# Optimization experiments

Hardware: AMD Instinct MI355X
Metric: run time of the kernel (lower is better)

## Reference

```python
import jax, jax.numpy as jnp
import numpy as np

N = 50000
E = 1600000
F_IN = 256
DIMS = 64
N_CLS = 16
R = 8


def glorot(key, shape):
    fan = shape[-2] + shape[-1] if len(shape) >= 2 else shape[-1] * 2
    std = jnp.sqrt(6.0 / fan)
    return jax.random.uniform(key, shape, jnp.float32, -std, std)


def setup_inputs() -> dict:
    key = jax.random.key(0)
    ks = jax.random.split(key, 12)
    x = jax.random.normal(ks[0], (N, F_IN), jnp.float32)
    edge_index = jax.random.randint(ks[1], (2, E), 0, N)
    edge_weight = jax.random.uniform(ks[2], (E,), jnp.float32)
    edge_color = jax.random.randint(ks[3], (E,), 0, R)
    W1 = glorot(ks[4], (R, F_IN, DIMS))
    atten1 = glorot(ks[5], (R, 2 * DIMS))
    root1 = glorot(ks[6], (F_IN, DIMS))
    bias1 = jnp.zeros((DIMS,), jnp.float32)
    W2 = glorot(ks[7], (R, DIMS, N_CLS))
    atten2 = glorot(ks[8], (R, 2 * N_CLS))
    root2 = glorot(ks[9], (DIMS, N_CLS))
    bias2 = jnp.zeros((N_CLS,), jnp.float32)
    return dict(x=x, edge_index=edge_index, edge_weight=edge_weight,
                edge_color=edge_color, W1=W1, atten1=atten1, root1=root1,
                bias1=bias1, W2=W2, atten2=atten2, root2=root2, bias2=bias2)


def wrgat_conv(x, src, dst, ew, ec, W, atten, root, bias):
    # x: [N, f_in]; W: [R, f_in, d]; atten: [R, 2d]
    d = W.shape[-1]
    xr = jnp.einsum('nf,rfd->rnd', x, W)            # [R, N, d] per-relation projection
    xi = xr[ec, dst]                                 # [E, d] dst (x_i)
    xj = xr[ec, src]                                 # [E, d] src (x_j)
    a_i = atten[:, :d][ec]                           # [E, d]
    a_j = atten[:, d:][ec]
    s = jnp.sum(a_i * xi + a_j * xj, axis=-1)        # [E]
    s = jax.nn.leaky_relu(s, 0.2)
    # segment softmax over (relation, destination) groups
    seg = ec * N + dst                               # [E], each edge belongs to one relation
    nseg = R * N
    m = jax.ops.segment_max(s, seg, num_segments=nseg)
    m = jnp.where(jnp.isfinite(m), m, 0.0)           # empty segments -> 0
    e = jnp.exp(s - m[seg])
    denom = jax.ops.segment_sum(e, seg, num_segments=nseg)
    alpha = e / jnp.maximum(denom[seg], 1e-16)
    msg = (alpha * ew)[:, None] * xj                 # [E, d]
    summed = jax.ops.segment_sum(msg, seg, num_segments=nseg).reshape(R, N, d)
    cnt = jax.ops.segment_sum(jnp.ones_like(ew), seg, num_segments=nseg).reshape(R, N, 1)
    out = (summed / jnp.maximum(cnt, 1.0)).sum(axis=0)  # mean aggr per relation, summed over relations
    return out + x @ root + bias


def reference(x, edge_index, edge_weight, edge_color, W1, atten1, root1, bias1,
              W2, atten2, root2, bias2):
    src, dst = edge_index[0], edge_index[1]          # PyG flow source_to_target: x_j=src, x_i=dst
    h = wrgat_conv(x, src, dst, edge_weight, edge_color, W1, atten1, root1, bias1)
    h = jax.nn.relu(h)                               # dropout p=0 -> identity
    h = wrgat_conv(h, src, dst, edge_weight, edge_color, W2, atten2, root2, bias2)
    return jax.nn.log_softmax(h, axis=1)
```

## Files before the change

### kernel.cpp

```cpp
#include <hip/hip_runtime.h>
#include <math.h>

#define N_NODES 50000
#define N_EDGES 1600000
#define F_IN    256
#define DIMS    64
#define N_CLS   16
#define R_REL   8
#define CAP     96

#define PROJ_BLKS 3519
#define CSR_BLKS  3125
#define FRONT_BLKS (PROJ_BLKS + CSR_BLKS)

typedef short bf16x8 __attribute__((ext_vector_type(8)));
typedef float f32x4  __attribute__((ext_vector_type(4)));
typedef unsigned int u32;
typedef const __attribute__((address_space(1))) u32* gas_ptr;
typedef __attribute__((address_space(3))) u32* las_ptr;

__device__ __forceinline__ void async16(const void* g, void* l) {
    __builtin_amdgcn_global_load_lds((gas_ptr)g, (las_ptr)l, 16, 0, 0);
}

__device__ __forceinline__ unsigned short f2bf(float f) {
    unsigned u = __float_as_uint(f);
    unsigned r = (u + 0x7fffu + ((u >> 16) & 1u)) >> 16;
    return (unsigned short)r;
}
__device__ __forceinline__ float bf2f(unsigned short u) {
    return __uint_as_float(((unsigned)u) << 16);
}

__global__ __launch_bounds__(256) void cvt_kernel(
        const float* __restrict__ x, ushort* __restrict__ xb,
        const float* __restrict__ W1, const float* __restrict__ root1,
        ushort* __restrict__ wt1) {
    const int bid = blockIdx.x, t = threadIdx.x;
    if (bid < 12500) {
        int i4 = bid * 256 + t;
        float4 v = ((const float4*)x)[i4];
        ushort4 o;
        o.x = f2bf(v.x); o.y = f2bf(v.y); o.z = f2bf(v.z); o.w = f2bf(v.w);
        ((ushort4*)xb)[i4] = o;
    } else {
        int idx = (bid - 12500) * 256 + t;
        int r = idx >> 14, rem = idx & 16383;
        int n = rem >> 8, k = rem & 255;
        float v = (r < 8) ? W1[((size_t)r * F_IN + k) * DIMS + n]
                          : root1[(size_t)k * DIMS + n];
        wt1[idx] = f2bf(v);
    }
}

#define BM 128
__global__ __launch_bounds__(256, 6) void front_kernel(
        const ushort* __restrict__ xb, const ushort* __restrict__ wt1,
        const float* __restrict__ at1,
        ushort* __restrict__ xr1b, float* __restrict__ hroot,
        float* __restrict__ si1, float* __restrict__ sj1,
        const int* __restrict__ ei, const int* __restrict__ ecol,
        const float* __restrict__ ew, int* __restrict__ fill,
        unsigned long long* __restrict__ rec) {
    __shared__ ushort xs[BM * 64];
    const int bid = blockIdx.x;
    const int t = threadIdx.x;

    int pb = -1, cb = -1;
    if (bid < 2 * CSR_BLKS) { if (bid & 1) cb = bid >> 1; else pb = bid >> 1; }
    else pb = CSR_BLKS + (bid - 2 * CSR_BLKS);

    if (cb >= 0) {
        int idx = cb * 256 + t;
        int2  s2 = ((const int2*)ei)[idx];
        int2  d2 = ((const int2*)(ei + N_EDGES))[idx];
        int2  c2 = ((const int2*)ecol)[idx];
        float2 w2 = ((const float2*)ew)[idx];
        int p0 = atomicAdd(&fill[d2.x], 1);
        int p1 = atomicAdd(&fill[d2.y], 1);
        unsigned long long r0 =
            ((unsigned long long)__float_as_uint(w2.x) << 32)
            | (unsigned)(s2.x | (c2.x << 16));
        unsigned long long r1 =
            ((unsigned long long)__float_as_uint(w2.y) << 32)
            | (unsigned)(s2.y | (c2.y << 16));
        int i0 = (p0 < CAP) ? d2.x * CAP + p0 : N_NODES * CAP;
        int i1 = (p1 < CAP) ? d2.y * CAP + p1 : N_NODES * CAP;
        __builtin_nontemporal_store(r0, &rec[i0]);
        __builtin_nontemporal_store(r1, &rec[i1]);
        return;
    }

    const int r = pb / 391;
    const int node0 = (pb % 391) * BM;
    const ushort* wrow = wt1 + (size_t)r * 64 * 256;

    const int w = t >> 6, lane = t & 63;
    const int lane15 = lane & 15, quad = lane >> 4;
    const int row0 = w * 32 + lane15;
    const int sw0 = row0 & 7;

    f32x4 acc[2][4];
    #pragma unroll
    for (int a = 0; a < 2; ++a)
        #pragma unroll
        for (int b = 0; b < 4; ++b)
            acc[a][b] = (f32x4){0.f, 0.f, 0.f, 0.f};

    for (int s = 0; s < 4; ++s) {
        __syncthreads();
        #pragma unroll
        for (int c = 0; c < 4; ++c) {
            int slot = c * 256 + t;
            int row = slot >> 3, k8p = slot & 7;
            int k8 = k8p ^ (row & 7);
            int node = node0 + row;
            if (node >= N_NODES) node = N_NODES - 1;
            async16(&xb[(size_t)node * 256 + s * 64 + k8 * 8],
                    &xs[(c * 256 + w * 64) * 8]);
        }
        __syncthreads();
        #pragma unroll
        for (int kk = 0; kk < 2; ++kk) {
            int k8 = kk * 4 + quad;
            int aidx = row0 * 64 + ((k8 ^ sw0) << 3);
            bf16x8 a0 = *(const bf16x8*)&xs[aidx];
            bf16x8 a1 = *(const bf16x8*)&xs[aidx + 16 * 64];
            int kg = s * 64 + kk * 32 + quad * 8;
            #pragma unroll
            for (int nt = 0; nt < 4; ++nt) {
                bf16x8 b = *(const bf16x8*)&wrow[(size_t)(nt * 16 + lane15) * 256 + kg];
                acc[0][nt] = __builtin_amdgcn_mfma_f32_16x16x32_bf16(a0, b, acc[0][nt], 0, 0, 0);
                acc[1][nt] = __builtin_amdgcn_mfma_f32_16x16x32_bf16(a1, b, acc[1][nt], 0, 0, 0);
            }
        }
    }

    const float* at = at1 + r * 128;
    #pragma unroll
    for (int mt = 0; mt < 2; ++mt) {
        float pi[4] = {0.f, 0.f, 0.f, 0.f};
        float pj[4] = {0.f, 0.f, 0.f, 0.f};
        #pragma unroll
        for (int nt = 0; nt < 4; ++nt) {
            int gcol = nt * 16 + lane15;
            float ai = 0.f, aj = 0.f;
            if (r < 8) { ai = at[gcol]; aj = at[64 + gcol]; }
            #pragma unroll
            for (int reg = 0; reg < 4; ++reg) {
                float v = acc[mt][nt][reg];
                int grow = node0 + w * 32 + mt * 16 + quad * 4 + reg;
                if (grow < N_NODES) {
                    if (r < 8)
                        xr1b[((size_t)r * N_NODES + grow) * 64 + gcol] = f2bf(v);
                    else
                        hroot[(size_t)grow * 64 + gcol] = v;
                }
                pi[reg] += ai * v;
                pj[reg] += aj * v;
            }
        }
        if (r < 8) {
            #pragma unroll
            for (int reg = 0; reg < 4; ++reg) {
                float s_ = pi[reg], u_ = pj[reg];
                #pragma unroll
                for (int off = 1; off < 16; off <<= 1) {
                    s_ += __shfl_xor(s_, off, 64);
                    u_ += __shfl_xor(u_, off, 64);
                }
                if (lane15 == 0) {
                    int grow = node0 + w * 32 + mt * 16 + quad * 4 + reg;
                    if (grow < N_NODES) {
                        si1[r * N_NODES + grow] = s_;
                        sj1[r * N_NODES + grow] = u_;
                    }
                }
            }
        }
    }
}

__global__ __launch_bounds__(256) void agg1s_kernel(
        const unsigned long long* __restrict__ rec, const int* __restrict__ fill,
        const float* __restrict__ si, const float* __restrict__ sj,
        const ushort* __restrict__ xr1b, const float* __restrict__ hroot,
        const float* __restrict__ bias1, float* __restrict__ h) {
    __shared__ int   esrc[4][CAP];
    __shared__ float ecoef[4][CAP];
    __shared__ float sden[4][8];
    __shared__ int   scnt[4][8];
    __shared__ float ssi[4][8];
    const int t = threadIdx.x;
    const int w = t >> 6, lane = t & 63;
    const int d = blockIdx.x * 4 + w;
    if (lane < 8) {
        sden[w][lane] = 0.f; scnt[w][lane] = 0;
        ssi[w][lane] = si[lane * N_NODES + d];
    }
    const int n = min(fill[d], CAP);
    const int base = d * CAP;
    float ex[2] = {0.f, 0.f}, ww[2] = {0.f, 0.f};
    int cc[2] = {0, 0};
    #pragma unroll
    for (int ii = 0; ii < 2; ++ii) {
        int i = lane + ii * 64;
        if (i < n) {
            unsigned long long rv = rec[base + i];
            int px = (int)(unsigned)rv;
            int s = px & 0xffff, c = (px >> 16) & 0x7fff;
            esrc[w][i] = px;
            float sc = ssi[w][c] + sj[c * N_NODES + s];
            sc = sc > 0.f ? sc : 0.2f * sc;
            float e = __expf(sc);
            ex[ii] = e; cc[ii] = c; ww[ii] = __uint_as_float((unsigned)(rv >> 32));
            atomicAdd(&sden[w][c], e);
            atomicAdd(&scnt[w][c], 1);
        }
    }
    #pragma unroll
    for (int ii = 0; ii < 2; ++ii) {
        int i = lane + ii * 64;
        if (i < n)
            ecoef[w][i] = ex[ii] / fmaxf(sden[w][cc[ii]], 1e-16f)
                          * ww[ii] / (float)scnt[w][cc[ii]];
    }
    const int sub = lane >> 5;
    const int l31 = lane & 31;
    float ax[8] = {0.f,0.f,0.f,0.f,0.f,0.f,0.f,0.f};
    float ay[8] = {0.f,0.f,0.f,0.f,0.f,0.f,0.f,0.f};
    int i0 = 0;
    for (; i0 + 16 <= n; i0 += 16) {
        u32 rv[8]; float cf[8];
        #pragma unroll
        for (int u = 0; u < 8; ++u) {
            int e = i0 + 2 * u + sub;
            int p = esrc[w][e];
            cf[u] = ecoef[w][e];
            int row = (p >> 16) * N_NODES + (p & 0xffff);
            rv[u] = *(const u32*)&xr1b[(size_t)row * 64 + 2 * l31];
        }
        #pragma unroll
        for (int u = 0; u < 8; ++u) {
            ax[u] += cf[u] * bf2f((unsigned short)(rv[u] & 0xffffu));
            ay[u] += cf[u] * bf2f((unsigned short)(rv[u] >> 16));
        }
    }
    for (int e = i0 + sub; e < n; e += 2) {
        int p = esrc[w][e];
        float c = ecoef[w][e];
        int row = (p >> 16) * N_NODES + (p & 0xffff);
        u32 v = *(const u32*)&xr1b[(size_t)row * 64 + 2 * l31];
        ax[0] += c * bf2f((unsigned short)(v & 0xffffu));
        ay[0] += c * bf2f((unsigned short)(v >> 16));
    }
    float sx = ((ax[0] + ax[1]) + (ax[2] + ax[3])) + ((ax[4] + ax[5]) + (ax[6] + ax[7]));
    float sy = ((ay[0] + ay[1]) + (ay[2] + ay[3])) + ((ay[4] + ay[5]) + (ay[6] + ay[7]));
    sx += __shfl_xor(sx, 32, 64);
    sy += __shfl_xor(sy, 32, 64);
    if (sub == 0) {
        float2 hr = *(const float2*)&hroot[(size_t)d * 64 + 2 * l31];
        float2 bi = *(const float2*)&bias1[2 * l31];
        float2 o;
        o.x = fmaxf(sx + hr.x + bi.x, 0.f);
        o.y = fmaxf(sy + hr.y + bi.y, 0.f);
        *(float2*)&h[(size_t)d * 64 + 2 * l31] = o;
    }
}

__global__ __launch_bounds__(256) void proj2_kernel(
        const float* __restrict__ h, const float* __restrict__ W2,
        const float* __restrict__ atten2, const float* __restrict__ root2,
        ushort* __restrict__ xr2b, float* __restrict__ si2,
        float* __restrict__ sj2, float* __restrict__ hroot2) {
    __shared__ float w2sh[8][64][16];
    __shared__ float a2sh[8][32];
    __shared__ float hsh[32][65];
    const int t = threadIdx.x;
    for (int i = t; i < R_REL * DIMS * N_CLS; i += 256)
        w2sh[i >> 10][(i >> 4) & 63][i & 15] = W2[i];
    if (t < R_REL * 2 * N_CLS) a2sh[t >> 5][t & 31] = atten2[t];
    const int node0 = blockIdx.x * 32;
    for (int i = t; i < 32 * 64; i += 256) {
        int nn = i >> 6, kk = i & 63;
        int node = node0 + nn;
        hsh[nn][kk] = (node < N_NODES) ? h[(size_t)node * 64 + kk] : 0.f;
    }
    __syncthreads();
    const int nl = t & 31, r = t >> 5;
    const int node = node0 + nl;
    float acc[16] = {};
    #pragma unroll 4
    for (int k = 0; k < 64; ++k) {
        float hv = hsh[nl][k];
        #pragma unroll
        for (int c = 0; c < 16; ++c) acc[c] += hv * w2sh[r][k][c];
    }
    if (node < N_NODES) {
        float si = 0.f, sj = 0.f;
        size_t base = ((size_t)r * N_NODES + node) * 16;
        #pragma unroll
        for (int c = 0; c < 16; ++c) {
            si += a2sh[r][c] * acc[c];
            sj += a2sh[r][16 + c] * acc[c];
        }
        #pragma unroll
        for (int c4 = 0; c4 < 4; ++c4) {
            ushort4 o;
            o.x = f2bf(acc[c4 * 4 + 0]); o.y = f2bf(acc[c4 * 4 + 1]);
            o.z = f2bf(acc[c4 * 4 + 2]); o.w = f2bf(acc[c4 * 4 + 3]);
            *(ushort4*)&xr2b[base + c4 * 4] = o;
        }
        si2[r * N_NODES + node] = si;
        sj2[r * N_NODES + node] = sj;
    }
    const int nn2 = t >> 3, cc0 = (t & 7) * 2;
    const int node2 = node0 + nn2;
    float h0 = 0.f, h1 = 0.f;
    #pragma unroll 8
    for (int k = 0; k < 64; ++k) {
        float hv = hsh[nn2][k];
        float2 rv = *(const float2*)&root2[(size_t)k * 16 + cc0];
        h0 += hv * rv.x; h1 += hv * rv.y;
    }
    if (node2 < N_NODES) {
        float2 o2; o2.x = h0; o2.y = h1;
        *(float2*)&hroot2[(size_t)node2 * 16 + cc0] = o2;
    }
}

__global__ __launch_bounds__(256) void agg2s_kernel(
        const unsigned long long* __restrict__ rec, const int* __restrict__ fill,
        const float* __restrict__ si, const float* __restrict__ sj,
        const ushort* __restrict__ xr2b, const float* __restrict__ hroot2,
        const float* __restrict__ bias2, float* __restrict__ out) {
    __shared__ int   esrc[4][CAP];
    __shared__ float ecoef[4][CAP];
    __shared__ float sden[4][8];
    __shared__ int   scnt[4][8];
    __shared__ float ssi[4][8];
    const int t = threadIdx.x;
    const int w = t >> 6, lane = t & 63;
    const int d = blockIdx.x * 4 + w;
    if (lane < 8) {
        sden[w][lane] = 0.f; scnt[w][lane] = 0;
        ssi[w][lane] = si[lane * N_NODES + d];
    }
    const int n = min(fill[d], CAP);
    const int base = d * CAP;
    float ex[2] = {0.f, 0.f}, ww[2] = {0.f, 0.f};
    int cc[2] = {0, 0};
    #pragma unroll
    for (int ii = 0; ii < 2; ++ii) {
        int i = lane + ii * 64;
        if (i < n) {
            unsigned long long rv = rec[base + i];
            int px = (int)(unsigned)rv;
            int s = px & 0xffff, c = (px >> 16) & 0x7fff;
            esrc[w][i] = px;
            float sc = ssi[w][c] + sj[c * N_NODES + s];
            sc = sc > 0.f ? sc : 0.2f * sc;
            float e = __expf(sc);
            ex[ii] = e; cc[ii] = c; ww[ii] = __uint_as_float((unsigned)(rv >> 32));
            atomicAdd(&sden[w][c], e);
            atomicAdd(&scnt[w][c], 1);
        }
    }
    #pragma unroll
    for (int ii = 0; ii < 2; ++ii) {
        int i = lane + ii * 64;
        if (i < n)
            ecoef[w][i] = ex[ii] / fmaxf(sden[w][cc[ii]], 1e-16f)
                          * ww[ii] / (float)scnt[w][cc[ii]];
    }
    const int sub = lane >> 3, cl = lane & 7, c0 = cl * 2;
    float a0x = 0.f, a0y = 0.f, a1x = 0.f, a1y = 0.f;
    int i = sub;
    for (; i + 8 < n; i += 16) {
        int p0 = esrc[w][i], p1 = esrc[w][i + 8];
        float f0 = ecoef[w][i], f1 = ecoef[w][i + 8];
        int r0 = (p0 >> 16) * N_NODES + (p0 & 0xffff);
        int r1 = (p1 >> 16) * N_NODES + (p1 & 0xffff);
        u32 v0 = *(const u32*)&xr2b[(size_t)r0 * 16 + c0];
        u32 v1 = *(const u32*)&xr2b[(size_t)r1 * 16 + c0];
        a0x += f0 * bf2f((unsigned short)(v0 & 0xffffu));
        a0y += f0 * bf2f((unsigned short)(v0 >> 16));
        a1x += f1 * bf2f((unsigned short)(v1 & 0xffffu));
        a1y += f1 * bf2f((unsigned short)(v1 >> 16));
    }
    for (; i < n; i += 8) {
        int p = esrc[w][i];
        float f = ecoef[w][i];
        int r0 = (p >> 16) * N_NODES + (p & 0xffff);
        u32 v = *(const u32*)&xr2b[(size_t)r0 * 16 + c0];
        a0x += f * bf2f((unsigned short)(v & 0xffffu));
        a0y += f * bf2f((unsigned short)(v >> 16));
    }
    float accx = a0x + a1x, accy = a0y + a1y;
    accx += __shfl_xor(accx, 8, 64);  accy += __shfl_xor(accy, 8, 64);
    accx += __shfl_xor(accx, 16, 64); accy += __shfl_xor(accy, 16, 64);
    accx += __shfl_xor(accx, 32, 64); accy += __shfl_xor(accy, 32, 64);
    if (sub == 0) {
        float2 hr = *(const float2*)&hroot2[(size_t)d * 16 + c0];
        accx += hr.x + bias2[c0];
        accy += hr.y + bias2[c0 + 1];
        float m = fmaxf(accx, accy);
        #pragma unroll
        for (int off = 1; off < 8; off <<= 1) m = fmaxf(m, __shfl_xor(m, off, 64));
        float e0 = expf(accx - m), e1 = expf(accy - m);
        float ssum = e0 + e1;
        #pragma unroll
        for (int off = 1; off < 8; off <<= 1) ssum += __shfl_xor(ssum, off, 64);
        float lse = m + logf(ssum);
        float2 o; o.x = accx - lse; o.y = accy - lse;
        *(float2*)&out[(size_t)d * 16 + c0] = o;
    }
}

extern "C" void kernel_launch(void* const* d_in, const int* in_sizes, int n_in,
                              void* d_out, int out_size, void* d_ws, size_t ws_size,
                              hipStream_t stream) {
    const float* x     = (const float*)d_in[0];
    const int*   ei    = (const int*)  d_in[1];
    const float* ew    = (const float*)d_in[2];
    const int*   ecol  = (const int*)  d_in[3];
    const float* W1    = (const float*)d_in[4];
    const float* at1   = (const float*)d_in[5];
    const float* root1 = (const float*)d_in[6];
    const float* b1    = (const float*)d_in[7];
    const float* W2    = (const float*)d_in[8];
    const float* at2   = (const float*)d_in[9];
    const float* root2 = (const float*)d_in[10];
    const float* b2    = (const float*)d_in[11];
    float* out = (float*)d_out;
    float* ws  = (float*)d_ws;

    ushort*   xb     = (ushort*)(ws + 0);
    ushort*   wt1    = (ushort*)(ws + 6400000);
    ushort*   xr1b   = (ushort*)(ws + 6480000);
    float*    hroot  = ws + 19280000;
    float*    hroot2 = ws + 19280000;
    ushort*   xr2b   = (ushort*)(ws + 22480000);
    float*    si1    = ws + 25680000;
    float*    sj1    = ws + 26080000;
    float*    si2    = ws + 26480000;
    float*    sj2    = ws + 26880000;
    int*      fill   = (int*)(ws + 27280000);
    float*    h      = ws + 27330000;
    unsigned long long* rec = (unsigned long long*)(ws + 30530000);

    hipMemsetAsync(fill, 0, (size_t)N_NODES * 4, stream);

    cvt_kernel<<<13076, 256, 0, stream>>>(x, xb, W1, root1, wt1);
    front_kernel<<<FRONT_BLKS, 256, 0, stream>>>(xb, wt1, at1, xr1b, hroot,
                                                 si1, sj1, ei, ecol, ew, fill, rec);
    agg1s_kernel<<<12500, 256, 0, stream>>>(rec, fill, si1, sj1, xr1b, hroot, b1, h);
    proj2_kernel<<<1563, 256, 0, stream>>>(h, W2, at2, root2, xr2b, si2, sj2, hroot2);
    agg2s_kernel<<<12500, 256, 0, stream>>>(rec, fill, si2, sj2, xr2b, hroot2, b2, out);
}
```

Baseline: 386.0 us.

## Aggregate raw hidden features per relation in layer 2, project after aggregation

Layer 1 now writes the hidden activations as bf16 instead of fp32. Layer 2 no longer materialises the per-relation projected table xr2b. Instead, agg2 gathers the bf16 hidden rows for each source, accumulates them per relation into shared memory with LDS atomics, and then multiplies each relation's accumulated vector by W2 before the log-softmax. This removes the 8x-expanded projection write and replaces it with a gather from a single 50000x64 bf16 table. The gather width grows from 16 to 64 features per edge, and the change adds LDS atomic contention and a per-node 8x64x16 matmul that reads W2 from global memory.

```diff
diff --git a/kernel.cpp b/kernel.cpp
--- a/kernel.cpp
+++ b/kernel.cpp
@@ -185,7 +185,7 @@
         const unsigned long long* __restrict__ rec, const int* __restrict__ fill,
         const float* __restrict__ si, const float* __restrict__ sj,
         const ushort* __restrict__ xr1b, const float* __restrict__ hroot,
-        const float* __restrict__ bias1, float* __restrict__ h) {
+        const float* __restrict__ bias1, ushort* __restrict__ hb) {
     __shared__ int   esrc[4][CAP];
     __shared__ float ecoef[4][CAP];
     __shared__ float sden[4][8];
@@ -261,18 +261,18 @@
     if (sub == 0) {
         float2 hr = *(const float2*)&hroot[(size_t)d * 64 + 2 * l31];
         float2 bi = *(const float2*)&bias1[2 * l31];
-        float2 o;
-        o.x = fmaxf(sx + hr.x + bi.x, 0.f);
-        o.y = fmaxf(sy + hr.y + bi.y, 0.f);
-        *(float2*)&h[(size_t)d * 64 + 2 * l31] = o;
+        float ox = fmaxf(sx + hr.x + bi.x, 0.f);
+        float oy = fmaxf(sy + hr.y + bi.y, 0.f);
+        u32 pk = ((u32)f2bf(oy) << 16) | (u32)f2bf(ox);
+        *(u32*)&hb[(size_t)d * 64 + 2 * l31] = pk;
     }
 }
 
 __global__ __launch_bounds__(256) void proj2_kernel(
-        const float* __restrict__ h, const float* __restrict__ W2,
+        const ushort* __restrict__ hb, const float* __restrict__ W2,
         const float* __restrict__ atten2, const float* __restrict__ root2,
-        ushort* __restrict__ xr2b, float* __restrict__ si2,
-        float* __restrict__ sj2, float* __restrict__ hroot2) {
+        float* __restrict__ si2, float* __restrict__ sj2,
+        float* __restrict__ hroot2) {
     __shared__ float w2sh[8][64][16];
     __shared__ float a2sh[8][32];
     __shared__ float hsh[32][65];
@@ -284,7 +284,7 @@
     for (int i = t; i < 32 * 64; i += 256) {
         int nn = i >> 6, kk = i & 63;
         int node = node0 + nn;
-        hsh[nn][kk] = (node < N_NODES) ? h[(size_t)node * 64 + kk] : 0.f;
+        hsh[nn][kk] = (node < N_NODES) ? bf2f(hb[(size_t)node * 64 + kk]) : 0.f;
     }
     __syncthreads();
     const int nl = t & 31, r = t >> 5;
@@ -298,18 +298,10 @@
     }
     if (node < N_NODES) {
         float si = 0.f, sj = 0.f;
-        size_t base = ((size_t)r * N_NODES + node) * 16;
         #pragma unroll
         for (int c = 0; c < 16; ++c) {
             si += a2sh[r][c] * acc[c];
             sj += a2sh[r][16 + c] * acc[c];
-        }
-        #pragma unroll
-        for (int c4 = 0; c4 < 4; ++c4) {
-            ushort4 o;
-            o.x = f2bf(acc[c4 * 4 + 0]); o.y = f2bf(acc[c4 * 4 + 1]);
-            o.z = f2bf(acc[c4 * 4 + 2]); o.w = f2bf(acc[c4 * 4 + 3]);
-            *(ushort4*)&xr2b[base + c4 * 4] = o;
         }
         si2[r * N_NODES + node] = si;
         sj2[r * N_NODES + node] = sj;
@@ -329,16 +321,18 @@
     }
 }
 
-__global__ __launch_bounds__(256) void agg2s_kernel(
+__global__ __launch_bounds__(256) void agg2h_kernel(
         const unsigned long long* __restrict__ rec, const int* __restrict__ fill,
         const float* __restrict__ si, const float* __restrict__ sj,
-        const ushort* __restrict__ xr2b, const float* __restrict__ hroot2,
-        const float* __restrict__ bias2, float* __restrict__ out) {
+        const ushort* __restrict__ hb, const float* __restrict__ hroot2,
+        const float* __restrict__ W2, const float* __restrict__ bias2,
+        float* __restrict__ out) {
     __shared__ int   esrc[4][CAP];
     __shared__ float ecoef[4][CAP];
     __shared__ float sden[4][8];
     __shared__ int   scnt[4][8];
     __shared__ float ssi[4][8];
+    __shared__ float A[4][8][64];
     const int t = threadIdx.x;
     const int w = t >> 6, lane = t & 63;
     const int d = blockIdx.x * 4 + w;
@@ -346,6 +340,8 @@
         sden[w][lane] = 0.f; scnt[w][lane] = 0;
         ssi[w][lane] = si[lane * N_NODES + d];
     }
+    #pragma unroll
+    for (int z = 0; z < 8; ++z) A[w][z][lane] = 0.f;
     const int n = min(fill[d], CAP);
     const int base = d * CAP;
     float ex[2] = {0.f, 0.f}, ww[2] = {0.f, 0.f};
@@ -373,47 +369,52 @@
             ecoef[w][i] = ex[ii] / fmaxf(sden[w][cc[ii]], 1e-16f)
                           * ww[ii] / (float)scnt[w][cc[ii]];
     }
-    const int sub = lane >> 3, cl = lane & 7, c0 = cl * 2;
-    float a0x = 0.f, a0y = 0.f, a1x = 0.f, a1y = 0.f;
-    int i = sub;
-    for (; i + 8 < n; i += 16) {
-        int p0 = esrc[w][i], p1 = esrc[w][i + 8];
-        float f0 = ecoef[w][i], f1 = ecoef[w][i + 8];
-        int r0 = (p0 >> 16) * N_NODES + (p0 & 0xffff);
-        int r1 = (p1 >> 16) * N_NODES + (p1 & 0xffff);
-        u32 v0 = *(const u32*)&xr2b[(size_t)r0 * 16 + c0];
-        u32 v1 = *(const u32*)&xr2b[(size_t)r1 * 16 + c0];
-        a0x += f0 * bf2f((unsigned short)(v0 & 0xffffu));
-        a0y += f0 * bf2f((unsigned short)(v0 >> 16));
-        a1x += f1 * bf2f((unsigned short)(v1 & 0xffffu));
-        a1y += f1 * bf2f((unsigned short)(v1 >> 16));
-    }
-    for (; i < n; i += 8) {
-        int p = esrc[w][i];
-        float f = ecoef[w][i];
-        int r0 = (p >> 16) * N_NODES + (p & 0xffff);
-        u32 v = *(const u32*)&xr2b[(size_t)r0 * 16 + c0];
-        a0x += f * bf2f((unsigned short)(v & 0xffffu));
-        a0y += f * bf2f((unsigned short)(v >> 16));
-    }
-    float accx = a0x + a1x, accy = a0y + a1y;
-    accx += __shfl_xor(accx, 8, 64);  accy += __shfl_xor(accy, 8, 64);
-    accx += __shfl_xor(accx, 16, 64); accy += __shfl_xor(accy, 16, 64);
-    accx += __shfl_xor(accx, 32, 64); accy += __shfl_xor(accy, 32, 64);
-    if (sub == 0) {
-        float2 hr = *(const float2*)&hroot2[(size_t)d * 16 + c0];
-        accx += hr.x + bias2[c0];
-        accy += hr.y + bias2[c0 + 1];
-        float m = fmaxf(accx, accy);
-        #pragma unroll
-        for (int off = 1; off < 8; off <<= 1) m = fmaxf(m, __shfl_xor(m, off, 64));
-        float e0 = expf(accx - m), e1 = expf(accy - m);
-        float ssum = e0 + e1;
-        #pragma unroll
-        for (int off = 1; off < 8; off <<= 1) ssum += __shfl_xor(ssum, off, 64);
-        float lse = m + logf(ssum);
-        float2 o; o.x = accx - lse; o.y = accy - lse;
-        *(float2*)&out[(size_t)d * 16 + c0] = o;
+    const int sub = lane >> 5, l31 = lane & 31;
+    int i0 = 0;
+    for (; i0 + 16 <= n; i0 += 16) {
+        u32 rv[8]; float cf[8]; int cb[8];
+        #pragma unroll
+        for (int u = 0; u < 8; ++u) {
+            int e = i0 + 2 * u + sub;
+            int p = esrc[w][e];
+            cf[u] = ecoef[w][e];
+            cb[u] = p >> 16;
+            rv[u] = *(const u32*)&hb[(size_t)(p & 0xffff) * 64 + 2 * l31];
+        }
+        #pragma unroll
+        for (int u = 0; u < 8; ++u) {
+            atomicAdd(&A[w][cb[u]][2 * l31],     cf[u] * bf2f((unsigned short)(rv[u] & 0xffffu)));
+            atomicAdd(&A[w][cb[u]][2 * l31 + 1], cf[u] * bf2f((unsigned short)(rv[u] >> 16)));
+        }
+    }
+    for (int e = i0 + sub; e < n; e += 2) {
+        int p = esrc[w][e];
+        float c = ecoef[w][e];
+        u32 v = *(const u32*)&hb[(size_t)(p & 0xffff) * 64 + 2 * l31];
+        atomicAdd(&A[w][p >> 16][2 * l31],     c * bf2f((unsigned short)(v & 0xffffu)));
+        atomicAdd(&A[w][p >> 16][2 * l31 + 1], c * bf2f((unsigned short)(v >> 16)));
+    }
+    const int s4 = lane >> 4, cd = lane & 15;
+    float lg = 0.f;
+    #pragma unroll
+    for (int ci = 0; ci < 2; ++ci) {
+        int c = s4 * 2 + ci;
+        #pragma unroll 8
+        for (int k = 0; k < 64; ++k)
+            lg += A[w][c][k] * W2[((size_t)c * 64 + k) * 16 + cd];
+    }
+    lg += __shfl_xor(lg, 16, 64);
+    lg += __shfl_xor(lg, 32, 64);
+    if (s4 == 0) {
+        lg += hroot2[(size_t)d * 16 + cd] + bias2[cd];
+        float m = lg;
+        #pragma unroll
+        for (int off = 8; off; off >>= 1) m = fmaxf(m, __shfl_xor(m, off, 16));
+        float e2 = expf(lg - m);
+        float ssum = e2;
+        #pragma unroll
+        for (int off = 8; off; off >>= 1) ssum += __shfl_xor(ssum, off, 16);
+        out[(size_t)d * 16 + cd] = lg - m - logf(ssum);
     }
 }
 
@@ -440,13 +441,12 @@
     ushort*   xr1b   = (ushort*)(ws + 6480000);
     float*    hroot  = ws + 19280000;
     float*    hroot2 = ws + 19280000;
-    ushort*   xr2b   = (ushort*)(ws + 22480000);
     float*    si1    = ws + 25680000;
     float*    sj1    = ws + 26080000;
     float*    si2    = ws + 26480000;
     float*    sj2    = ws + 26880000;
     int*      fill   = (int*)(ws + 27280000);
-    float*    h      = ws + 27330000;
+    ushort*   hb     = (ushort*)(ws + 27330000);
     unsigned long long* rec = (unsigned long long*)(ws + 30530000);
 
     hipMemsetAsync(fill, 0, (size_t)N_NODES * 4, stream);
@@ -454,7 +454,7 @@
     cvt_kernel<<<13076, 256, 0, stream>>>(x, xb, W1, root1, wt1);
     front_kernel<<<FRONT_BLKS, 256, 0, stream>>>(xb, wt1, at1, xr1b, hroot,
                                                  si1, sj1, ei, ecol, ew, fill, rec);
-    agg1s_kernel<<<12500, 256, 0, stream>>>(rec, fill, si1, sj1, xr1b, hroot, b1, h);
-    proj2_kernel<<<1563, 256, 0, stream>>>(h, W2, at2, root2, xr2b, si2, sj2, hroot2);
-    agg2s_kernel<<<12500, 256, 0, stream>>>(rec, fill, si2, sj2, xr2b, hroot2, b2, out);
-}
+    agg1s_kernel<<<12500, 256, 0, stream>>>(rec, fill, si1, sj1, xr1b, hroot, b1, hb);
+    proj2_kernel<<<1563, 256, 0, stream>>>(hb, W2, at2, root2, si2, sj2, hroot2);
+    agg2h_kernel<<<12500, 256, 0, stream>>>(rec, fill, si2, sj2, hb, hroot2, W2, b2, out);
+}
```

Result: slower. 908.3 us (+135.3%).
